# Kernel tuning notes

Measured on AMD Instinct MI355X. Metric: run time of the kernel, lower is better.

The kernel has to match this reference:

```python
import jax, jax.numpy as jnp
import numpy as np

NEG_SLOPE = 0.2
ZTOL = 1e-9
INF = 1e12


def _gat_forward(x, a, W, S):
    # x: [B,G,N], a: [P,E,2F], W: [P,E,F,G], S: [E,N,N]
    B, G, N = x.shape
    P, E, twoF = a.shape
    F = W.shape[2]
    # self-loops added ONLY for the attention mask (faithful to source:
    # learnAttentionGSO modifies S locally; graphAttention's final matmul uses original S)
    S_I = S + jnp.eye(N, dtype=S.dtype)[None]
    Wx = jnp.einsum('pefg,bgn->bpefn', W, x)  # [B,P,E,F,N]
    a1, a2 = a[..., :F], a[..., F:]
    s1 = jnp.einsum('pef,bpefn->bpen', a1, Wx)  # varies along j (columns)
    s2 = jnp.einsum('pef,bpefn->bpen', a2, Wx)  # varies along i (rows)
    e = s1[:, :, :, None, :] + s2[:, :, :, :, None]  # [B,P,E,N,N], e[...,i,j]
    e = jnp.where(e >= 0, e, NEG_SLOPE * e)  # leaky relu
    mask = (jnp.sum(jnp.abs(S_I), axis=0) > ZTOL).astype(x.dtype)  # [N,N]
    scores = e * mask - (1.0 - mask) * INF
    aij = jax.nn.softmax(scores, axis=-1) * mask  # [B,P,E,N,N]
    # y_i = sum_e sum_j s_ij^e * alpha_ij * W x_j  (original S, no self-loop)
    y = jnp.einsum('bpefm,bpemn->bpfn', Wx, S[None, None] * aij)  # [B,P,F,N]
    y = jax.nn.relu(y)
    # concatenate heads: [B,P,F,N] -> [B, P*F, N]
    return y.transpose(0, 3, 1, 2).reshape(B, N, P * F).transpose(0, 2, 1)


def setup_inputs() -> dict:
    key = jax.random.key(0)
    k1, k2, k3, k4, k5 = jax.random.split(key, 5)
    B, G, N, P, E, F = 4, 128, 2048, 4, 1, 64
    x = jax.random.normal(k1, (B, G, N), dtype=jnp.float32)
    stdv = 1.0 / np.sqrt(G * P)  # matches reset_parameters
    a = jax.random.uniform(k2, (P, E, 2 * F), jnp.float32, -stdv, stdv)
    W = jax.random.uniform(k3, (P, E, F, G), jnp.float32, -stdv, stdv)
    density = 0.05
    Svals = jax.random.normal(k4, (E, N, N), dtype=jnp.float32)
    Smask = (jax.random.uniform(k5, (E, N, N)) < density).astype(jnp.float32)
    S = Svals * Smask
    return {"x": x, "a": a, "W": W, "S": S}


def reference(x, a, W, S):
    return _gat_forward(x, a, W, S)
```

## Files before the change

kernel.cpp:

```cpp
#include <hip/hip_runtime.h>
#include <hip/hip_bf16.h>

typedef unsigned short u16;
typedef unsigned int u32;

#define NEG_SLOPE 0.2f
#define ZTOLF 1e-9f
#define CAP 256

typedef __attribute__((ext_vector_type(4))) float f32x4;
typedef __attribute__((ext_vector_type(8))) short bf16x8;

__device__ __forceinline__ float b2f(u16 v) {
  return __uint_as_float(((u32)v) << 16);
}
__device__ __forceinline__ u16 f2b(float f) {
  u32 u = __float_as_uint(f);
  return (u16)((u + 0x7fffu + ((u >> 16) & 1u)) >> 16);
}
__device__ __forceinline__ float ldin(const void* p, size_t i, int isbf) {
  return isbf ? b2f(((const u16*)p)[i]) : ((const float*)p)[i];
}

__global__ __launch_bounds__(256) void k_detect(const u32* __restrict__ xw,
                                                u32* __restrict__ flag,
                                                uint4* __restrict__ cnt_p4) {
  __shared__ u32 cnt_s[4];
  const int tid = threadIdx.x;
  const uint4 z = make_uint4(0u, 0u, 0u, 0u);
  for (int i = tid; i < 8192; i += 256) cnt_p4[i] = z;
  const u32 w = xw[tid];
  const u32 e = (w >> 7) & 0xffu;
  const int in = (e >= 118u && e <= 131u) ? 1 : 0;
  unsigned long long bal = __ballot(in);
  const int lane = tid & 63, wid = tid >> 6;
  if (lane == 0) cnt_s[wid] = (u32)__popcll(bal);
  __syncthreads();
  if (tid == 0) {
    u32 tot = cnt_s[0] + cnt_s[1] + cnt_s[2] + cnt_s[3];
    flag[0] = (tot >= 128u) ? 1u : 0u;
  }
}

__global__ __launch_bounds__(256) void k_wx(const void* __restrict__ x,
                                            const void* __restrict__ W,
                                            const void* __restrict__ a,
                                            u16* __restrict__ Wx,
                                            float* __restrict__ s1t,
                                            float* __restrict__ s2t,
                                            const u32* __restrict__ flag) {
  __shared__ float smem_f[64 * 68 + 64 * 64];
  const int isbf = (int)flag[0];
  const int tid = threadIdx.x;
  const int n0 = blockIdx.x * 64;
  const int bp = blockIdx.y;
  const int b = bp >> 2, p = bp & 3;

  if (isbf) {
    u16* XsT = (u16*)smem_f;
    const u16* xb = (const u16*)x + (size_t)b * 128 * 2048;
    const u16* Wb = (const u16*)W + (size_t)p * 64 * 128;
#pragma unroll
    for (int j = 0; j < 4; ++j) {
      const int idx = tid + j * 256;
      const int g = idx >> 3, ng = (idx & 7) * 8;
      uint4 pk = *(const uint4*)(xb + (size_t)g * 2048 + n0 + ng);
      u16 e[8];
      e[0] = (u16)(pk.x & 0xffffu); e[1] = (u16)(pk.x >> 16);
      e[2] = (u16)(pk.y & 0xffffu); e[3] = (u16)(pk.y >> 16);
      e[4] = (u16)(pk.z & 0xffffu); e[5] = (u16)(pk.z >> 16);
      e[6] = (u16)(pk.w & 0xffffu); e[7] = (u16)(pk.w >> 16);
#pragma unroll
      for (int i = 0; i < 8; ++i) XsT[(ng + i) * 136 + g] = e[i];
    }
    __syncthreads();
    const int lane = tid & 63, wv = tid >> 6;
    const int f0 = wv * 16;
    const int arow = lane & 15, kgrp = lane >> 4;
    f32x4 zero = {0.f, 0.f, 0.f, 0.f};
    f32x4 acc[4] = {zero, zero, zero, zero};
#pragma unroll
    for (int kb = 0; kb < 4; ++kb) {
      bf16x8 afrag = *(const bf16x8*)(Wb + (size_t)(f0 + arow) * 128 + kb * 32 + kgrp * 8);
#pragma unroll
      for (int t = 0; t < 4; ++t) {
        bf16x8 bfrag = *(const bf16x8*)&XsT[(t * 16 + arow) * 136 + kb * 32 + kgrp * 8];
        acc[t] = __builtin_amdgcn_mfma_f32_16x16x32_bf16(afrag, bfrag, acc[t], 0, 0, 0);
      }
    }
    float a1v[4], a2v[4];
#pragma unroll
    for (int v = 0; v < 4; ++v) {
      a1v[v] = b2f(((const u16*)a)[p * 128 + f0 + kgrp * 4 + v]);
      a2v[v] = b2f(((const u16*)a)[p * 128 + 64 + f0 + kgrp * 4 + v]);
    }
    __syncthreads();
    float* red1 = smem_f;
    float* red2 = smem_f + 64 * 17;
#pragma unroll
    for (int t = 0; t < 4; ++t) {
      const int n_l = t * 16 + arow;
      u32 lo = (u32)f2b(acc[t][0]) | ((u32)f2b(acc[t][1]) << 16);
      u32 hi = (u32)f2b(acc[t][2]) | ((u32)f2b(acc[t][3]) << 16);
      *(uint2*)(Wx + ((size_t)(bp * 2048 + n0 + n_l) * 64 + f0 + kgrp * 4)) = make_uint2(lo, hi);
      float p1 = a1v[0] * acc[t][0] + a1v[1] * acc[t][1] + a1v[2] * acc[t][2] + a1v[3] * acc[t][3];
      float p2 = a2v[0] * acc[t][0] + a2v[1] * acc[t][1] + a2v[2] * acc[t][2] + a2v[3] * acc[t][3];
      red1[n_l * 17 + wv * 4 + kgrp] = p1;
      red2[n_l * 17 + wv * 4 + kgrp] = p2;
    }
    __syncthreads();
    if (tid < 64) {
      float v1 = 0.f, v2 = 0.f;
#pragma unroll
      for (int k = 0; k < 16; ++k) {
        v1 += red1[tid * 17 + k];
        v2 += red2[tid * 17 + k];
      }
      s1t[(size_t)(n0 + tid) * 16 + bp] = v1;
      s2t[(size_t)(n0 + tid) * 16 + bp] = v2;
    }
    return;
  }

  float* Wt = smem_f;
  float* Xs = smem_f + 64 * 68;
  const int tn = tid & 15, tf = tid >> 4;
  float acc[4][4] = {{0.f}};
  const size_t Wbase = (size_t)p * 64 * 128;
  const size_t xbase = (size_t)b * 128 * 2048;
  for (int kt = 0; kt < 2; ++kt) {
    const int g0 = kt * 64;
#pragma unroll
    for (int j = 0; j < 16; ++j) {
      int idx = tid + j * 256;
      int f = idx >> 6, g = idx & 63;
      Wt[g * 68 + f] = ((const float*)W)[Wbase + (size_t)f * 128 + g0 + g];
    }
#pragma unroll
    for (int j = 0; j < 16; ++j) {
      int idx = tid + j * 256;
      int g = idx >> 6, nn = idx & 63;
      Xs[g * 64 + nn] = ((const float*)x)[xbase + (size_t)(g0 + g) * 2048 + n0 + nn];
    }
    __syncthreads();
#pragma unroll 4
    for (int g = 0; g < 64; ++g) {
      float4 wv = *(const float4*)&Wt[g * 68 + tf * 4];
      float4 xv = *(const float4*)&Xs[g * 64 + tn * 4];
      acc[0][0] += wv.x * xv.x; acc[0][1] += wv.x * xv.y; acc[0][2] += wv.x * xv.z; acc[0][3] += wv.x * xv.w;
      acc[1][0] += wv.y * xv.x; acc[1][1] += wv.y * xv.y; acc[1][2] += wv.y * xv.z; acc[1][3] += wv.y * xv.w;
      acc[2][0] += wv.z * xv.x; acc[2][1] += wv.z * xv.y; acc[2][2] += wv.z * xv.z; acc[2][3] += wv.z * xv.w;
      acc[3][0] += wv.w * xv.x; acc[3][1] += wv.w * xv.y; acc[3][2] += wv.w * xv.z; acc[3][3] += wv.w * xv.w;
    }
    __syncthreads();
  }
#pragma unroll
  for (int j = 0; j < 4; ++j) {
    int n = n0 + tn * 4 + j;
    u32 lo = (u32)f2b(acc[0][j]) | ((u32)f2b(acc[1][j]) << 16);
    u32 hi = (u32)f2b(acc[2][j]) | ((u32)f2b(acc[3][j]) << 16);
    *(uint2*)(Wx + ((size_t)(bp * 2048 + n) * 64 + tf * 4)) = make_uint2(lo, hi);
  }
  float a1v[4], a2v[4];
#pragma unroll
  for (int fi = 0; fi < 4; ++fi) {
    a1v[fi] = ((const float*)a)[(size_t)p * 128 + tf * 4 + fi];
    a2v[fi] = ((const float*)a)[(size_t)p * 128 + 64 + tf * 4 + fi];
  }
  float* red1 = Wt;
  float* red2 = Wt + 64 * 17;
#pragma unroll
  for (int j = 0; j < 4; ++j) {
    float p1 = a1v[0] * acc[0][j] + a1v[1] * acc[1][j] + a1v[2] * acc[2][j] + a1v[3] * acc[3][j];
    float p2 = a2v[0] * acc[0][j] + a2v[1] * acc[1][j] + a2v[2] * acc[2][j] + a2v[3] * acc[3][j];
    red1[(tn * 4 + j) * 17 + tf] = p1;
    red2[(tn * 4 + j) * 17 + tf] = p2;
  }
  __syncthreads();
  if (tid < 64) {
    float v1 = 0.f, v2 = 0.f;
#pragma unroll
    for (int k = 0; k < 16; ++k) {
      v1 += red1[tid * 17 + k];
      v2 += red2[tid * 17 + k];
    }
    s1t[(size_t)(n0 + tid) * 16 + bp] = v1;
    s2t[(size_t)(n0 + tid) * 16 + bp] = v2;
  }
}

__global__ __launch_bounds__(256) void k_csc(const void* __restrict__ S,
                                             u32* __restrict__ cnt_p,
                                             u32* __restrict__ col_m,
                                             float* __restrict__ col_v,
                                             const float* __restrict__ s1t,
                                             const float* __restrict__ s2t,
                                             float4* __restrict__ stat3,
                                             const u32* __restrict__ flag) {
  __shared__ u32 wsum[4];
  __shared__ u32 ls_n[CAP];
  __shared__ u32 c2s;
  __shared__ float red[256];
  __shared__ float Mred[16];
  const int isbf = (int)flag[0];
  const int m = blockIdx.x;
  const int tid = threadIdx.x;
  const int lane = tid & 63, wid = tid >> 6;
  const int n0 = tid * 8;
  float v[8];
  if (isbf) {
    uint4 pk = ((const uint4*)S)[(size_t)m * 256 + tid];
    u32 wv[4] = {pk.x, pk.y, pk.z, pk.w};
#pragma unroll
    for (int j = 0; j < 4; ++j) {
      v[2 * j]     = b2f((u16)(wv[j] & 0xffffu));
      v[2 * j + 1] = b2f((u16)(wv[j] >> 16));
    }
  } else {
    float4 f0 = ((const float4*)S)[(size_t)m * 512 + 2 * tid];
    float4 f1 = ((const float4*)S)[(size_t)m * 512 + 2 * tid + 1];
    v[0] = f0.x; v[1] = f0.y; v[2] = f0.z; v[3] = f0.w;
    v[4] = f1.x; v[5] = f1.y; v[6] = f1.z; v[7] = f1.w;
  }
  u32 rflags = 0, rc = 0;
#pragma unroll
  for (int j = 0; j < 8; ++j) {
    const int n = n0 + j;
    const float svd = (n == m) ? v[j] + 1.f : v[j];
    if (fabsf(svd) > ZTOLF) { rflags |= 1u << j; rc++; }
  }
  u32 inc = rc;
#pragma unroll
  for (int off = 1; off < 64; off <<= 1) {
    u32 y = __shfl_up(inc, off);
    if (lane >= off) inc += y;
  }
  if (lane == 63) wsum[wid] = inc;
  __syncthreads();
  u32 wbase = 0;
#pragma unroll
  for (int k = 0; k < 4; ++k) wbase += (k < wid) ? wsum[k] : 0u;
  u32 pos = wbase + inc - rc;
#pragma unroll
  for (int j = 0; j < 8; ++j) {
    if ((rflags >> j) & 1u) {
      if (pos < CAP) ls_n[pos] = (u32)(n0 + j);
      pos++;
    }
  }
  if (tid == 255) c2s = min(wbase + inc, (u32)CAP);
#pragma unroll
  for (int j = 0; j < 8; ++j) {
    const float sv = v[j];
    if (sv != 0.f) {
      const int n = n0 + j;
      u32 slot = atomicAdd(&cnt_p[(size_t)n * 16], 1u);
      if (slot < CAP) {
        col_m[(size_t)n * CAP + slot] = (u32)m;
        col_v[(size_t)n * CAP + slot] = sv;
      }
    }
  }
  __syncthreads();
  const int c2 = (int)c2s;
  const int bp = tid & 15, sub = tid >> 4;
  const float s2v = s2t[(size_t)m * 16 + bp];
  float ev[16];
  float mymax = -3e38f;
#pragma unroll
  for (int k = 0; k < 16; ++k) {
    const int i = sub + k * 16;
    float e = -3e38f;
    if (i < c2) {
      const int nn = (int)ls_n[i];
      float s1 = s1t[(size_t)nn * 16 + bp];
      e = s1 + s2v;
      e = e >= 0.f ? e : NEG_SLOPE * e;
    }
    ev[k] = e;
    mymax = fmaxf(mymax, e);
  }
  red[tid] = mymax;
  __syncthreads();
  if (tid < 16) {
    float M = -3e38f;
#pragma unroll
    for (int s = 0; s < 16; ++s) M = fmaxf(M, red[s * 16 + tid]);
    Mred[tid] = M;
  }
  __syncthreads();
  const float M = Mred[bp];
  float ssum = 0.f;
#pragma unroll
  for (int k = 0; k < 16; ++k) ssum += __expf(ev[k] - M);
  __syncthreads();
  red[tid] = ssum;
  __syncthreads();
  if (tid < 16) {
    float Sm = 0.f;
#pragma unroll
    for (int s = 0; s < 16; ++s) Sm += red[s * 16 + tid];
    const float Mv = Mred[tid];
    const bool any = (Mv > -1e38f);
    const float rmx = any ? Mv : 0.f;
    const float inv = any ? 1.f / Sm : 0.f;
    const float s2o = s2t[(size_t)m * 16 + tid];
    stat3[(size_t)m * 16 + tid] = make_float4(s2o, rmx, inv, 0.f);
  }
}

__global__ __launch_bounds__(256, 8) void k_out(const u16* __restrict__ Wx,
                                                const u32* __restrict__ cnt_p,
                                                const u32* __restrict__ col_m,
                                                const float* __restrict__ col_v,
                                                const float* __restrict__ s1t,
                                                const float4* __restrict__ stat3,
                                                void* __restrict__ out,
                                                const u32* __restrict__ flag) {
  __shared__ u32 lds_m[CAP];
  __shared__ float lds_v[CAP];
  __shared__ float lds_w[CAP * 4];
  __shared__ float lds_r[3 * 256];
  __shared__ float s1s4[4];
  const int isbf = (int)flag[0];
  const int tid = threadIdx.x;
  const int bid = blockIdx.x;
  const int xcd = bid & 7, lin = bid >> 3;
  const int bpg = xcd >> 1;
  const int n = ((xcd & 1) << 10) | lin;
  const int c = min((int)cnt_p[(size_t)n * 16], CAP);
  const int cpad = (c + 15) & ~15;
  if (tid < 4) s1s4[tid] = s1t[(size_t)n * 16 + bpg * 4 + tid];
  if (tid < cpad) {
    lds_m[tid] = (tid < c) ? col_m[(size_t)n * CAP + tid] : 0u;
    lds_v[tid] = (tid < c) ? col_v[(size_t)n * CAP + tid] : 0.f;
  }
  __syncthreads();
  const int totk = cpad * 4;
  for (int k = tid; k < totk; k += 256) {
    const int i = k >> 2, bp4 = k & 3;
    const int bp = bpg * 4 + bp4;
    float w = 0.f;
    if (i < c) {
      const int mm = (int)lds_m[i];
      const float sv = lds_v[i];
      const float svd = (mm == n) ? sv + 1.f : sv;
      if (fabsf(svd) > ZTOLF) {
        float4 s = stat3[(size_t)mm * 16 + bp];
        float e = s1s4[bp4] + s.x;
        e = e >= 0.f ? e : NEG_SLOPE * e;
        w = sv * __expf(e - s.y) * s.z;
      }
    }
    lds_w[k] = w;
  }
  __syncthreads();
  const int lane = tid & 63, h = tid >> 6;
  const int bp4 = lane >> 4, bp = bpg * 4 + bp4;
  const int f4 = lane & 15;
  const u16* wxp = Wx + (size_t)bp * (2048 * 64) + f4 * 4;
  float ac0 = 0.f, ac1 = 0.f, ac2 = 0.f, ac3 = 0.f;
  for (int base = h * 4; base < cpad; base += 16) {
    uint2 wd[4]; float ww[4];
#pragma unroll
    for (int j = 0; j < 4; ++j) {
      const int i = base + j;
      const int mm = (int)lds_m[i];
      wd[j] = *(const uint2*)(wxp + (size_t)mm * 64);
      ww[j] = lds_w[i * 4 + bp4];
    }
#pragma unroll
    for (int j = 0; j < 4; ++j) {
      const float w = ww[j];
      ac0 += w * b2f((u16)(wd[j].x & 0xffffu));
      ac1 += w * b2f((u16)(wd[j].x >> 16));
      ac2 += w * b2f((u16)(wd[j].y & 0xffffu));
      ac3 += w * b2f((u16)(wd[j].y >> 16));
    }
  }
  if (h > 0)
    *(float4*)&lds_r[(h - 1) * 256 + (bp4 * 16 + f4) * 4] = make_float4(ac0, ac1, ac2, ac3);
  __syncthreads();
  if (h == 0) {
#pragma unroll
    for (int q = 0; q < 3; ++q) {
      float4 r = *(const float4*)&lds_r[q * 256 + (bp4 * 16 + f4) * 4];
      ac0 += r.x; ac1 += r.y; ac2 += r.z; ac3 += r.w;
    }
    const float o0 = fmaxf(ac0, 0.f), o1 = fmaxf(ac1, 0.f);
    const float o2 = fmaxf(ac2, 0.f), o3 = fmaxf(ac3, 0.f);
    const size_t r0 = (size_t)(bp * 64 + f4 * 4);
    if (isbf) {
      u16* ob = (u16*)out;
      ob[(r0 + 0) * 2048 + n] = f2b(o0);
      ob[(r0 + 1) * 2048 + n] = f2b(o1);
      ob[(r0 + 2) * 2048 + n] = f2b(o2);
      ob[(r0 + 3) * 2048 + n] = f2b(o3);
    } else {
      float* of = (float*)out;
      of[(r0 + 0) * 2048 + n] = o0;
      of[(r0 + 1) * 2048 + n] = o1;
      of[(r0 + 2) * 2048 + n] = o2;
      of[(r0 + 3) * 2048 + n] = o3;
    }
  }
}

extern "C" void kernel_launch(void* const* d_in, const int* in_sizes, int n_in,
                              void* d_out, int out_size, void* d_ws, size_t ws_size,
                              hipStream_t stream) {
  const void* x = d_in[0];
  const void* a = d_in[1];
  const void* W = d_in[2];
  const void* S = d_in[3];

  char* ws = (char*)d_ws;
  u16* Wx      = (u16*)ws;
  float* s1t   = (float*)(ws + 4u * 1024 * 1024);
  float* s2t   = s1t + 2048 * 16;
  float4* stat3= (float4*)(s2t + 2048 * 16);
  u32* cnt_p   = (u32*)((char*)stat3 + 512u * 1024);
  u32* col_m   = cnt_p + 2048 * 16;
  float* col_v = (float*)(col_m + 2048 * CAP);
  u32* flag    = (u32*)(col_v + 2048 * CAP);

  k_detect<<<1, 256, 0, stream>>>((const u32*)x, flag, (uint4*)cnt_p);
  k_wx<<<dim3(32, 16), 256, 0, stream>>>(x, W, a, Wx, s1t, s2t, flag);
  k_csc<<<2048, 256, 0, stream>>>(S, cnt_p, col_m, col_v, s1t, s2t, stat3, flag);
  k_out<<<8192, 256, 0, stream>>>(Wx, cnt_p, col_m, col_v, s1t, stat3, d_out, flag);
}
```

Before: 139.3 us.

## Replace sparse CSC gather output kernel with dense MFMA attention-weighted matmul

Drops the atomic column-list build in k_csc and the per-column gather kernel. A new k_outd streams dense S tiles, computes the attention weights for each 64x64 tile into LDS as bf16, and multiplies them with a transposed Wx using bf16 MFMA. Wx is now written transposed so the MFMA B fragments load contiguously. This removes atomics, scattered gathers and the 8192-block launch in exchange for reading the full dense S per bp (16 times over) and doing dense compute on a 5%-dense matrix. Only 512 blocks are launched.

```diff
diff --git a/kernel.cpp b/kernel.cpp
--- a/kernel.cpp
+++ b/kernel.cpp
@@ -18,17 +18,11 @@
   u32 u = __float_as_uint(f);
   return (u16)((u + 0x7fffu + ((u >> 16) & 1u)) >> 16);
 }
-__device__ __forceinline__ float ldin(const void* p, size_t i, int isbf) {
-  return isbf ? b2f(((const u16*)p)[i]) : ((const float*)p)[i];
-}
 
 __global__ __launch_bounds__(256) void k_detect(const u32* __restrict__ xw,
-                                                u32* __restrict__ flag,
-                                                uint4* __restrict__ cnt_p4) {
+                                                u32* __restrict__ flag) {
   __shared__ u32 cnt_s[4];
   const int tid = threadIdx.x;
-  const uint4 z = make_uint4(0u, 0u, 0u, 0u);
-  for (int i = tid; i < 8192; i += 256) cnt_p4[i] = z;
   const u32 w = xw[tid];
   const u32 e = (w >> 7) & 0xffu;
   const int in = (e >= 118u && e <= 131u) ? 1 : 0;
@@ -45,7 +39,7 @@
 __global__ __launch_bounds__(256) void k_wx(const void* __restrict__ x,
                                             const void* __restrict__ W,
                                             const void* __restrict__ a,
-                                            u16* __restrict__ Wx,
+                                            u16* __restrict__ WxT,
                                             float* __restrict__ s1t,
                                             float* __restrict__ s2t,
                                             const u32* __restrict__ flag) {
@@ -100,9 +94,9 @@
 #pragma unroll
     for (int t = 0; t < 4; ++t) {
       const int n_l = t * 16 + arow;
-      u32 lo = (u32)f2b(acc[t][0]) | ((u32)f2b(acc[t][1]) << 16);
-      u32 hi = (u32)f2b(acc[t][2]) | ((u32)f2b(acc[t][3]) << 16);
-      *(uint2*)(Wx + ((size_t)(bp * 2048 + n0 + n_l) * 64 + f0 + kgrp * 4)) = make_uint2(lo, hi);
+#pragma unroll
+      for (int v = 0; v < 4; ++v)
+        WxT[(size_t)(bp * 64 + f0 + kgrp * 4 + v) * 2048 + n0 + n_l] = f2b(acc[t][v]);
       float p1 = a1v[0] * acc[t][0] + a1v[1] * acc[t][1] + a1v[2] * acc[t][2] + a1v[3] * acc[t][3];
       float p2 = a2v[0] * acc[t][0] + a2v[1] * acc[t][1] + a2v[2] * acc[t][2] + a2v[3] * acc[t][3];
       red1[n_l * 17 + wv * 4 + kgrp] = p1;
@@ -156,10 +150,10 @@
   }
 #pragma unroll
   for (int j = 0; j < 4; ++j) {
-    int n = n0 + tn * 4 + j;
-    u32 lo = (u32)f2b(acc[0][j]) | ((u32)f2b(acc[1][j]) << 16);
-    u32 hi = (u32)f2b(acc[2][j]) | ((u32)f2b(acc[3][j]) << 16);
-    *(uint2*)(Wx + ((size_t)(bp * 2048 + n) * 64 + tf * 4)) = make_uint2(lo, hi);
+    const int n = n0 + tn * 4 + j;
+#pragma unroll
+    for (int i = 0; i < 4; ++i)
+      WxT[(size_t)(bp * 64 + tf * 4 + i) * 2048 + n] = f2b(acc[i][j]);
   }
   float a1v[4], a2v[4];
 #pragma unroll
@@ -190,9 +184,6 @@
 }
 
 __global__ __launch_bounds__(256) void k_csc(const void* __restrict__ S,
-                                             u32* __restrict__ cnt_p,
-                                             u32* __restrict__ col_m,
-                                             float* __restrict__ col_v,
                                              const float* __restrict__ s1t,
                                              const float* __restrict__ s2t,
                                              float4* __restrict__ stat3,
@@ -249,18 +240,6 @@
     }
   }
   if (tid == 255) c2s = min(wbase + inc, (u32)CAP);
-#pragma unroll
-  for (int j = 0; j < 8; ++j) {
-    const float sv = v[j];
-    if (sv != 0.f) {
-      const int n = n0 + j;
-      u32 slot = atomicAdd(&cnt_p[(size_t)n * 16], 1u);
-      if (slot < CAP) {
-        col_m[(size_t)n * CAP + slot] = (u32)m;
-        col_v[(size_t)n * CAP + slot] = sv;
-      }
-    }
-  }
   __syncthreads();
   const int c2 = (int)c2s;
   const int bp = tid & 15, sub = tid >> 4;
@@ -285,7 +264,7 @@
   if (tid < 16) {
     float M = -3e38f;
 #pragma unroll
-    for (int s = 0; s < 16; ++s) M = fmaxf(M, red[s * 16 + tid]);
+    for (int ss = 0; ss < 16; ++ss) M = fmaxf(M, red[ss * 16 + tid]);
     Mred[tid] = M;
   }
   __syncthreads();
@@ -299,7 +278,7 @@
   if (tid < 16) {
     float Sm = 0.f;
 #pragma unroll
-    for (int s = 0; s < 16; ++s) Sm += red[s * 16 + tid];
+    for (int ss = 0; ss < 16; ++ss) Sm += red[ss * 16 + tid];
     const float Mv = Mred[tid];
     const bool any = (Mv > -1e38f);
     const float rmx = any ? Mv : 0.f;
@@ -309,100 +288,95 @@
   }
 }
 
-__global__ __launch_bounds__(256, 8) void k_out(const u16* __restrict__ Wx,
-                                                const u32* __restrict__ cnt_p,
-                                                const u32* __restrict__ col_m,
-                                                const float* __restrict__ col_v,
-                                                const float* __restrict__ s1t,
-                                                const float4* __restrict__ stat3,
-                                                void* __restrict__ out,
-                                                const u32* __restrict__ flag) {
-  __shared__ u32 lds_m[CAP];
-  __shared__ float lds_v[CAP];
-  __shared__ float lds_w[CAP * 4];
-  __shared__ float lds_r[3 * 256];
-  __shared__ float s1s4[4];
+__global__ __launch_bounds__(256, 8) void k_outd(const u16* __restrict__ WxT,
+                                                 const void* __restrict__ S,
+                                                 const float* __restrict__ s1t,
+                                                 const float4* __restrict__ stat3,
+                                                 void* __restrict__ out,
+                                                 const u32* __restrict__ flag) {
+  __shared__ u16 wT[64 * 72];
+  __shared__ float s1s[64];
   const int isbf = (int)flag[0];
   const int tid = threadIdx.x;
   const int bid = blockIdx.x;
-  const int xcd = bid & 7, lin = bid >> 3;
-  const int bpg = xcd >> 1;
-  const int n = ((xcd & 1) << 10) | lin;
-  const int c = min((int)cnt_p[(size_t)n * 16], CAP);
-  const int cpad = (c + 15) & ~15;
-  if (tid < 4) s1s4[tid] = s1t[(size_t)n * 16 + bpg * 4 + tid];
-  if (tid < cpad) {
-    lds_m[tid] = (tid < c) ? col_m[(size_t)n * CAP + tid] : 0u;
-    lds_v[tid] = (tid < c) ? col_v[(size_t)n * CAP + tid] : 0.f;
-  }
-  __syncthreads();
-  const int totk = cpad * 4;
-  for (int k = tid; k < totk; k += 256) {
-    const int i = k >> 2, bp4 = k & 3;
-    const int bp = bpg * 4 + bp4;
-    float w = 0.f;
-    if (i < c) {
-      const int mm = (int)lds_m[i];
-      const float sv = lds_v[i];
-      const float svd = (mm == n) ? sv + 1.f : sv;
-      if (fabsf(svd) > ZTOLF) {
-        float4 s = stat3[(size_t)mm * 16 + bp];
-        float e = s1s4[bp4] + s.x;
-        e = e >= 0.f ? e : NEG_SLOPE * e;
-        w = sv * __expf(e - s.y) * s.z;
+  const int nt = bid & 31, bp = bid >> 5;
+  const int n0 = nt * 64;
+  if (tid < 64) s1s[tid] = s1t[(size_t)(n0 + tid) * 16 + bp];
+  const int lane = tid & 63, wv = tid >> 6;
+  const int arow = lane & 15, kgrp = lane >> 4;
+  const int f0 = wv * 16;
+  const int mw = tid >> 3;
+  const int n8 = (tid & 7) * 8;
+  f32x4 zero = {0.f, 0.f, 0.f, 0.f};
+  f32x4 acc[4] = {zero, zero, zero, zero};
+  const u16* S16 = (const u16*)S;
+  const float* S32 = (const float*)S;
+  __syncthreads();
+  for (int m0 = 0; m0 < 2048; m0 += 64) {
+#pragma unroll
+    for (int pass = 0; pass < 2; ++pass) {
+      const int m_l = pass * 32 + mw;
+      const int m = m0 + m_l;
+      float sv[8];
+      if (isbf) {
+        uint4 pk = *(const uint4*)(S16 + (size_t)m * 2048 + n0 + n8);
+        sv[0] = b2f((u16)(pk.x & 0xffffu)); sv[1] = b2f((u16)(pk.x >> 16));
+        sv[2] = b2f((u16)(pk.y & 0xffffu)); sv[3] = b2f((u16)(pk.y >> 16));
+        sv[4] = b2f((u16)(pk.z & 0xffffu)); sv[5] = b2f((u16)(pk.z >> 16));
+        sv[6] = b2f((u16)(pk.w & 0xffffu)); sv[7] = b2f((u16)(pk.w >> 16));
+      } else {
+        float4 a4 = *(const float4*)(S32 + (size_t)m * 2048 + n0 + n8);
+        float4 b4 = *(const float4*)(S32 + (size_t)m * 2048 + n0 + n8 + 4);
+        sv[0] = a4.x; sv[1] = a4.y; sv[2] = a4.z; sv[3] = a4.w;
+        sv[4] = b4.x; sv[5] = b4.y; sv[6] = b4.z; sv[7] = b4.w;
       }
-    }
-    lds_w[k] = w;
-  }
-  __syncthreads();
-  const int lane = tid & 63, h = tid >> 6;
-  const int bp4 = lane >> 4, bp = bpg * 4 + bp4;
-  const int f4 = lane & 15;
-  const u16* wxp = Wx + (size_t)bp * (2048 * 64) + f4 * 4;
-  float ac0 = 0.f, ac1 = 0.f, ac2 = 0.f, ac3 = 0.f;
-  for (int base = h * 4; base < cpad; base += 16) {
-    uint2 wd[4]; float ww[4];
-#pragma unroll
-    for (int j = 0; j < 4; ++j) {
-      const int i = base + j;
-      const int mm = (int)lds_m[i];
-      wd[j] = *(const uint2*)(wxp + (size_t)mm * 64);
-      ww[j] = lds_w[i * 4 + bp4];
-    }
-#pragma unroll
-    for (int j = 0; j < 4; ++j) {
-      const float w = ww[j];
-      ac0 += w * b2f((u16)(wd[j].x & 0xffffu));
-      ac1 += w * b2f((u16)(wd[j].x >> 16));
-      ac2 += w * b2f((u16)(wd[j].y & 0xffffu));
-      ac3 += w * b2f((u16)(wd[j].y >> 16));
-    }
-  }
-  if (h > 0)
-    *(float4*)&lds_r[(h - 1) * 256 + (bp4 * 16 + f4) * 4] = make_float4(ac0, ac1, ac2, ac3);
-  __syncthreads();
-  if (h == 0) {
-#pragma unroll
-    for (int q = 0; q < 3; ++q) {
-      float4 r = *(const float4*)&lds_r[q * 256 + (bp4 * 16 + f4) * 4];
-      ac0 += r.x; ac1 += r.y; ac2 += r.z; ac3 += r.w;
-    }
-    const float o0 = fmaxf(ac0, 0.f), o1 = fmaxf(ac1, 0.f);
-    const float o2 = fmaxf(ac2, 0.f), o3 = fmaxf(ac3, 0.f);
-    const size_t r0 = (size_t)(bp * 64 + f4 * 4);
-    if (isbf) {
-      u16* ob = (u16*)out;
-      ob[(r0 + 0) * 2048 + n] = f2b(o0);
-      ob[(r0 + 1) * 2048 + n] = f2b(o1);
-      ob[(r0 + 2) * 2048 + n] = f2b(o2);
-      ob[(r0 + 3) * 2048 + n] = f2b(o3);
-    } else {
-      float* of = (float*)out;
-      of[(r0 + 0) * 2048 + n] = o0;
-      of[(r0 + 1) * 2048 + n] = o1;
-      of[(r0 + 2) * 2048 + n] = o2;
-      of[(r0 + 3) * 2048 + n] = o3;
-    }
+      const float4 st = stat3[(size_t)m * 16 + bp];
+#pragma unroll
+      for (int j = 0; j < 8; ++j) {
+        const int n = n0 + n8 + j;
+        const float svd = (m == n) ? sv[j] + 1.f : sv[j];
+        float w = 0.f;
+        if (fabsf(svd) > ZTOLF) {
+          float e = s1s[n8 + j] + st.x;
+          e = e >= 0.f ? e : NEG_SLOPE * e;
+          w = sv[j] * __expf(e - st.y) * st.z;
+        }
+        wT[(n8 + j) * 72 + m_l] = f2b(w);
+      }
+    }
+    __syncthreads();
+#pragma unroll
+    for (int kb = 0; kb < 2; ++kb) {
+      bf16x8 bfrag = *(const bf16x8*)(WxT + (size_t)(bp * 64 + f0 + arow) * 2048 + m0 + kb * 32 + kgrp * 8);
+#pragma unroll
+      for (int t = 0; t < 4; ++t) {
+        bf16x8 afrag = *(const bf16x8*)&wT[(t * 16 + arow) * 72 + kb * 32 + kgrp * 8];
+        acc[t] = __builtin_amdgcn_mfma_f32_16x16x32_bf16(afrag, bfrag, acc[t], 0, 0, 0);
+      }
+    }
+    __syncthreads();
+  }
+  if (isbf) {
+#pragma unroll
+    for (int t = 0; t < 4; ++t)
+#pragma unroll
+      for (int v = 0; v < 4; ++v)
+        wT[(f0 + arow) * 72 + t * 16 + kgrp * 4 + v] = f2b(fmaxf(acc[t][v], 0.f));
+    __syncthreads();
+    const int f = tid >> 2, q = tid & 3;
+    const u32* src = (const u32*)&wT[f * 72 + q * 16];
+    u16* ob = (u16*)out;
+    uint4 lo = make_uint4(src[0], src[1], src[2], src[3]);
+    uint4 hi = make_uint4(src[4], src[5], src[6], src[7]);
+    *(uint4*)(ob + (size_t)(bp * 64 + f) * 2048 + n0 + q * 16) = lo;
+    *(uint4*)(ob + (size_t)(bp * 64 + f) * 2048 + n0 + q * 16 + 8) = hi;
+  } else {
+    float* of = (float*)out;
+#pragma unroll
+    for (int t = 0; t < 4; ++t)
+#pragma unroll
+      for (int v = 0; v < 4; ++v)
+        of[(size_t)(bp * 64 + f0 + arow) * 2048 + n0 + t * 16 + kgrp * 4 + v] = fmaxf(acc[t][v], 0.f);
   }
 }
 
@@ -415,17 +389,14 @@
   const void* S = d_in[3];
 
   char* ws = (char*)d_ws;
-  u16* Wx      = (u16*)ws;
+  u16* WxT     = (u16*)ws;
   float* s1t   = (float*)(ws + 4u * 1024 * 1024);
   float* s2t   = s1t + 2048 * 16;
   float4* stat3= (float4*)(s2t + 2048 * 16);
-  u32* cnt_p   = (u32*)((char*)stat3 + 512u * 1024);
-  u32* col_m   = cnt_p + 2048 * 16;
-  float* col_v = (float*)(col_m + 2048 * CAP);
-  u32* flag    = (u32*)(col_v + 2048 * CAP);
-
-  k_detect<<<1, 256, 0, stream>>>((const u32*)x, flag, (uint4*)cnt_p);
-  k_wx<<<dim3(32, 16), 256, 0, stream>>>(x, W, a, Wx, s1t, s2t, flag);
-  k_csc<<<2048, 256, 0, stream>>>(S, cnt_p, col_m, col_v, s1t, s2t, stat3, flag);
-  k_out<<<8192, 256, 0, stream>>>(Wx, cnt_p, col_m, col_v, s1t, stat3, d_out, flag);
-}
+  u32* flag    = (u32*)((char*)stat3 + 512u * 1024);
+
+  k_detect<<<1, 256, 0, stream>>>((const u32*)x, flag);
+  k_wx<<<dim3(32, 16), 256, 0, stream>>>(x, W, a, WxT, s1t, s2t, flag);
+  k_csc<<<2048, 256, 0, stream>>>(S, s1t, s2t, stat3, flag);
+  k_outd<<<512, 256, 0, stream>>>(WxT, S, s1t, stat3, d_out, flag);
+}
```

After: 193.4 us. +38.8%, slower.
